# Optimization experiments

Measured on AMD Instinct MI355X. Metric: run time of the kernel, lower is better.

Reference implementation:

```python
import jax, jax.numpy as jnp
import numpy as np
from jax import lax

BETA = 0.95
THRESHOLD = 1.0
B, T, D_IN, D_OUT = 128, 512, 512, 512


def setup_inputs() -> dict:
    key = jax.random.key(0)
    k1, k2, k3 = jax.random.split(key, 3)
    x_seq = jax.random.normal(k1, (B, T, D_IN), dtype=jnp.float32)
    W = jax.random.normal(k2, (D_OUT, D_IN), dtype=jnp.float32) * (1.0 / np.sqrt(D_IN))
    b = jax.random.normal(k3, (D_OUT,), dtype=jnp.float32) * 0.01
    return {"x_seq": x_seq, "W": W, "b": b}


def reference(x_seq, W, b):
    # Batch the linear across all timesteps: [B,T,D_in] @ [D_out,D_in]^T -> [B,T,D_out]
    currents = jnp.einsum('bti,oi->bto', x_seq, W) + b

    def step(mem, cur):  # mem: [B, D_out], cur: [B, D_out]
        mem = BETA * mem + cur
        spk = (mem > THRESHOLD).astype(mem.dtype)
        return mem - spk * THRESHOLD, spk

    mem0 = jnp.zeros((x_seq.shape[0], W.shape[0]), dtype=x_seq.dtype)
    _, spikes_tbd = lax.scan(step, mem0, jnp.swapaxes(currents, 0, 1))  # [T,B,D]
    spikes = jnp.swapaxes(spikes_tbd, 0, 1)  # [B,T,D]
    return spikes, spikes.sum()
```

## Files before the change

### kernel.cpp

```cpp
#include <hip/hip_runtime.h>
#include <hip/hip_bf16.h>

#define M_TOT 65536
#define K_DIM 512
#define N_DIM 512
#define T_STEPS 512
#define BETA 0.95f

#define BM 128
#define BN 128
#define BK 64

typedef __attribute__((ext_vector_type(8))) short bf16x8;
typedef __attribute__((ext_vector_type(4))) float f32x4;

static __device__ __forceinline__ unsigned short f2bf(float f) {
    __hip_bfloat16 h = __float2bfloat16(f);
    return __builtin_bit_cast(unsigned short, h);
}

__global__ __launch_bounds__(256) void gemm_currents(
    const float* __restrict__ X,
    const float* __restrict__ W,
    const float* __restrict__ bias,
    float* __restrict__ C)
{
    __shared__ unsigned short Xs[BM][BK];
    __shared__ unsigned short Ws[BN][BK];

    const int lin  = blockIdx.x;
    const int swz  = (lin & 7) * 256 + (lin >> 3);
    const int mtile = swz >> 2;
    const int ntile = swz & 3;

    const int tid  = threadIdx.x;
    const int lane = tid & 63;
    const int wave = tid >> 6;
    const int wr = wave >> 1;
    const int wc = wave & 1;

    const int row0 = mtile * BM;
    const int col0 = ntile * BN;

    f32x4 acc[4][4] = {};

    const int sr0 = tid >> 4;
    const int skg = (tid & 15) << 2;

    for (int k0 = 0; k0 < K_DIM; k0 += BK) {
        #pragma unroll
        for (int i = 0; i < 8; ++i) {
            int r  = sr0 + i * 16;
            int kgs = skg ^ ((r & 7) << 3);
            float4 xv = *(const float4*)(X + (size_t)(row0 + r) * K_DIM + k0 + skg);
            float4 wv = *(const float4*)(W + (size_t)(col0 + r) * K_DIM + k0 + skg);
            ushort4 xb, wb;
            xb.x = f2bf(xv.x); xb.y = f2bf(xv.y); xb.z = f2bf(xv.z); xb.w = f2bf(xv.w);
            wb.x = f2bf(wv.x); wb.y = f2bf(wv.y); wb.z = f2bf(wv.z); wb.w = f2bf(wv.w);
            *(ushort4*)(&Xs[r][kgs]) = xb;
            *(ushort4*)(&Ws[r][kgs]) = wb;
        }
        __syncthreads();

        const int frow = lane & 15;
        const int cblk = lane >> 4;
        #pragma unroll
        for (int kh = 0; kh < 2; ++kh) {
            bf16x8 afr[4], bfr[4];
            #pragma unroll
            for (int m = 0; m < 4; ++m) {
                int row = wr * 64 + m * 16 + frow;
                int c = (kh * 4 + cblk) ^ (row & 7);
                afr[m] = *(const bf16x8*)(&Xs[row][c * 8]);
            }
            #pragma unroll
            for (int n = 0; n < 4; ++n) {
                int row = wc * 64 + n * 16 + frow;
                int c = (kh * 4 + cblk) ^ (row & 7);
                bfr[n] = *(const bf16x8*)(&Ws[row][c * 8]);
            }
            #pragma unroll
            for (int m = 0; m < 4; ++m)
                #pragma unroll
                for (int n = 0; n < 4; ++n)
                    acc[m][n] = __builtin_amdgcn_mfma_f32_16x16x32_bf16(
                        afr[m], bfr[n], acc[m][n], 0, 0, 0);
        }
        __syncthreads();
    }

    const int crow_base = (lane >> 4) * 4;
    const int ccol = lane & 15;
    #pragma unroll
    for (int n = 0; n < 4; ++n) {
        int col = col0 + wc * 64 + n * 16 + ccol;
        float bv = bias[col];
        #pragma unroll
        for (int m = 0; m < 4; ++m) {
            int rowb = row0 + wr * 64 + m * 16 + crow_base;
            #pragma unroll
            for (int r = 0; r < 4; ++r) {
                C[(size_t)(rowb + r) * N_DIM + col] = acc[m][n][r] + bv;
            }
        }
    }
}

__global__ void zero_sum(float* s) { *s = 0.0f; }

__global__ __launch_bounds__(256) void lif_scan(
    float* __restrict__ C,
    float* __restrict__ sum_out)
{
    const int idx = blockIdx.x * 256 + threadIdx.x;
    float* p = C + (size_t)(idx >> 9) * (T_STEPS * N_DIM) + (idx & 511);

    float mem = 0.0f;
    int count = 0;
    float a[8], b[8];

    #pragma unroll
    for (int j = 0; j < 8; ++j)
        a[j] = __builtin_nontemporal_load(p + (size_t)j * N_DIM);

    for (int t = 0; t < T_STEPS; t += 16) {
        #pragma unroll
        for (int j = 0; j < 8; ++j)
            b[j] = __builtin_nontemporal_load(p + (size_t)(t + 8 + j) * N_DIM);
        #pragma unroll
        for (int j = 0; j < 8; ++j) {
            mem = BETA * mem + a[j];
            float spk = (mem > 1.0f) ? 1.0f : 0.0f;
            mem -= spk;
            __builtin_nontemporal_store(spk, p + (size_t)(t + j) * N_DIM);
            count += (int)spk;
        }
        if (t + 16 < T_STEPS) {
            #pragma unroll
            for (int j = 0; j < 8; ++j)
                a[j] = __builtin_nontemporal_load(p + (size_t)(t + 16 + j) * N_DIM);
        }
        #pragma unroll
        for (int j = 0; j < 8; ++j) {
            mem = BETA * mem + b[j];
            float spk = (mem > 1.0f) ? 1.0f : 0.0f;
            mem -= spk;
            __builtin_nontemporal_store(spk, p + (size_t)(t + 8 + j) * N_DIM);
            count += (int)spk;
        }
    }

    #pragma unroll
    for (int off = 32; off > 0; off >>= 1)
        count += __shfl_down(count, off);
    __shared__ int wsum[4];
    if ((threadIdx.x & 63) == 0) wsum[threadIdx.x >> 6] = count;
    __syncthreads();
    if (threadIdx.x == 0) {
        int tot = wsum[0] + wsum[1] + wsum[2] + wsum[3];
        atomicAdd(sum_out, (float)tot);
    }
}

extern "C" void kernel_launch(void* const* d_in, const int* in_sizes, int n_in,
                              void* d_out, int out_size, void* d_ws, size_t ws_size,
                              hipStream_t stream) {
    const float* X    = (const float*)d_in[0];
    const float* W    = (const float*)d_in[1];
    const float* bias = (const float*)d_in[2];
    float* out = (float*)d_out;

    gemm_currents<<<(M_TOT / BM) * (N_DIM / BN), 256, 0, stream>>>(X, W, bias, out);
    zero_sum<<<1, 1, 0, stream>>>(out + (size_t)M_TOT * N_DIM);
    lif_scan<<<M_TOT / 256, 256, 0, stream>>>(out, out + (size_t)M_TOT * N_DIM);
}
```

Baseline: 333.3 us.

## Double-buffer GEMM LDS tiles with register prefetch, fold sum zeroing, deepen scan prefetch

The GEMM now keeps two LDS buffers. The next K tile is loaded from global into registers while MFMAs run on the current buffer, which removes one barrier per iteration and hides load latency. Zeroing of the sum slot moves into the GEMM kernel, dropping a separate launch. The LIF scan prefetches 16 timesteps per half instead of 8 and uses plain loads instead of nontemporal ones. The cost is higher register and LDS use, and launch_bounds(256,2) may constrain allocation.

```diff
diff --git a/kernel.cpp b/kernel.cpp
--- a/kernel.cpp
+++ b/kernel.cpp
@@ -19,14 +19,31 @@
     return __builtin_bit_cast(unsigned short, h);
 }
 
-__global__ __launch_bounds__(256) void gemm_currents(
+static __device__ __forceinline__ void stage_tiles(
+    unsigned short (*__restrict__ Xs)[BK], unsigned short (*__restrict__ Ws)[BK],
+    const float4* xr, const float4* wv, int sr0, int skg)
+{
+    #pragma unroll
+    for (int i = 0; i < 8; ++i) {
+        int r   = sr0 + i * 16;
+        int kgs = skg ^ ((r & 7) << 3);
+        ushort4 xb, wb;
+        xb.x = f2bf(xr[i].x); xb.y = f2bf(xr[i].y); xb.z = f2bf(xr[i].z); xb.w = f2bf(xr[i].w);
+        wb.x = f2bf(wv[i].x); wb.y = f2bf(wv[i].y); wb.z = f2bf(wv[i].z); wb.w = f2bf(wv[i].w);
+        *(ushort4*)(&Xs[r][kgs]) = xb;
+        *(ushort4*)(&Ws[r][kgs]) = wb;
+    }
+}
+
+__global__ __launch_bounds__(256, 2) void gemm_currents(
     const float* __restrict__ X,
     const float* __restrict__ W,
     const float* __restrict__ bias,
-    float* __restrict__ C)
+    float* __restrict__ C,
+    float* __restrict__ sum_out)
 {
-    __shared__ unsigned short Xs[BM][BK];
-    __shared__ unsigned short Ws[BN][BK];
+    __shared__ unsigned short Xs[2][BM][BK];
+    __shared__ unsigned short Ws[2][BN][BK];
 
     const int lin  = blockIdx.x;
     const int swz  = (lin & 7) * 256 + (lin >> 3);
@@ -39,6 +56,8 @@
     const int wr = wave >> 1;
     const int wc = wave & 1;
 
+    if (lin == 0 && tid == 0) *sum_out = 0.0f;
+
     const int row0 = mtile * BM;
     const int col0 = ntile * BN;
 
@@ -46,24 +65,37 @@
 
     const int sr0 = tid >> 4;
     const int skg = (tid & 15) << 2;
-
-    for (int k0 = 0; k0 < K_DIM; k0 += BK) {
-        #pragma unroll
-        for (int i = 0; i < 8; ++i) {
-            int r  = sr0 + i * 16;
-            int kgs = skg ^ ((r & 7) << 3);
-            float4 xv = *(const float4*)(X + (size_t)(row0 + r) * K_DIM + k0 + skg);
-            float4 wv = *(const float4*)(W + (size_t)(col0 + r) * K_DIM + k0 + skg);
-            ushort4 xb, wb;
-            xb.x = f2bf(xv.x); xb.y = f2bf(xv.y); xb.z = f2bf(xv.z); xb.w = f2bf(xv.w);
-            wb.x = f2bf(wv.x); wb.y = f2bf(wv.y); wb.z = f2bf(wv.z); wb.w = f2bf(wv.w);
-            *(ushort4*)(&Xs[r][kgs]) = xb;
-            *(ushort4*)(&Ws[r][kgs]) = wb;
-        }
+    const float* xbase = X + (size_t)row0 * K_DIM + skg;
+    const float* wbase = W + (size_t)col0 * K_DIM + skg;
+
+    float4 xr[8], wv[8];
+
+    #pragma unroll
+    for (int i = 0; i < 8; ++i) {
+        int r = sr0 + i * 16;
+        xr[i] = *(const float4*)(xbase + (size_t)r * K_DIM);
+        wv[i] = *(const float4*)(wbase + (size_t)r * K_DIM);
+    }
+    stage_tiles(Xs[0], Ws[0], xr, wv, sr0, skg);
+
+    const int frow = lane & 15;
+    const int cblk = lane >> 4;
+
+    for (int t = 0; t < 8; ++t) {
         __syncthreads();
 
-        const int frow = lane & 15;
-        const int cblk = lane >> 4;
+        if (t < 7) {
+            const int k0n = (t + 1) * BK;
+            #pragma unroll
+            for (int i = 0; i < 8; ++i) {
+                int r = sr0 + i * 16;
+                xr[i] = *(const float4*)(xbase + (size_t)r * K_DIM + k0n);
+                wv[i] = *(const float4*)(wbase + (size_t)r * K_DIM + k0n);
+            }
+        }
+
+        unsigned short (*Xb)[BK] = Xs[t & 1];
+        unsigned short (*Wb)[BK] = Ws[t & 1];
         #pragma unroll
         for (int kh = 0; kh < 2; ++kh) {
             bf16x8 afr[4], bfr[4];
@@ -71,13 +103,13 @@
             for (int m = 0; m < 4; ++m) {
                 int row = wr * 64 + m * 16 + frow;
                 int c = (kh * 4 + cblk) ^ (row & 7);
-                afr[m] = *(const bf16x8*)(&Xs[row][c * 8]);
+                afr[m] = *(const bf16x8*)(&Xb[row][c * 8]);
             }
             #pragma unroll
             for (int n = 0; n < 4; ++n) {
                 int row = wc * 64 + n * 16 + frow;
                 int c = (kh * 4 + cblk) ^ (row & 7);
-                bfr[n] = *(const bf16x8*)(&Ws[row][c * 8]);
+                bfr[n] = *(const bf16x8*)(&Wb[row][c * 8]);
             }
             #pragma unroll
             for (int m = 0; m < 4; ++m)
@@ -86,7 +118,9 @@
                     acc[m][n] = __builtin_amdgcn_mfma_f32_16x16x32_bf16(
                         afr[m], bfr[n], acc[m][n], 0, 0, 0);
         }
-        __syncthreads();
+
+        if (t < 7)
+            stage_tiles(Xs[(t + 1) & 1], Ws[(t + 1) & 1], xr, wv, sr0, skg);
     }
 
     const int crow_base = (lane >> 4) * 4;
@@ -105,8 +139,6 @@
         }
     }
 }
-
-__global__ void zero_sum(float* s) { *s = 0.0f; }
 
 __global__ __launch_bounds__(256) void lif_scan(
     float* __restrict__ C,
@@ -117,35 +149,35 @@
 
     float mem = 0.0f;
     int count = 0;
-    float a[8], b[8];
-
-    #pragma unroll
-    for (int j = 0; j < 8; ++j)
-        a[j] = __builtin_nontemporal_load(p + (size_t)j * N_DIM);
-
-    for (int t = 0; t < T_STEPS; t += 16) {
-        #pragma unroll
-        for (int j = 0; j < 8; ++j)
-            b[j] = __builtin_nontemporal_load(p + (size_t)(t + 8 + j) * N_DIM);
-        #pragma unroll
-        for (int j = 0; j < 8; ++j) {
+    float a[16], b[16];
+
+    #pragma unroll
+    for (int j = 0; j < 16; ++j)
+        a[j] = p[(size_t)j * N_DIM];
+
+    for (int t = 0; t < T_STEPS; t += 32) {
+        #pragma unroll
+        for (int j = 0; j < 16; ++j)
+            b[j] = p[(size_t)(t + 16 + j) * N_DIM];
+        #pragma unroll
+        for (int j = 0; j < 16; ++j) {
             mem = BETA * mem + a[j];
             float spk = (mem > 1.0f) ? 1.0f : 0.0f;
             mem -= spk;
             __builtin_nontemporal_store(spk, p + (size_t)(t + j) * N_DIM);
             count += (int)spk;
         }
-        if (t + 16 < T_STEPS) {
-            #pragma unroll
-            for (int j = 0; j < 8; ++j)
-                a[j] = __builtin_nontemporal_load(p + (size_t)(t + 16 + j) * N_DIM);
-        }
-        #pragma unroll
-        for (int j = 0; j < 8; ++j) {
+        if (t + 32 < T_STEPS) {
+            #pragma unroll
+            for (int j = 0; j < 16; ++j)
+                a[j] = p[(size_t)(t + 32 + j) * N_DIM];
+        }
+        #pragma unroll
+        for (int j = 0; j < 16; ++j) {
             mem = BETA * mem + b[j];
             float spk = (mem > 1.0f) ? 1.0f : 0.0f;
             mem -= spk;
-            __builtin_nontemporal_store(spk, p + (size_t)(t + 8 + j) * N_DIM);
+            __builtin_nontemporal_store(spk, p + (size_t)(t + 16 + j) * N_DIM);
             count += (int)spk;
         }
     }
@@ -169,8 +201,8 @@
     const float* W    = (const float*)d_in[1];
     const float* bias = (const float*)d_in[2];
     float* out = (float*)d_out;
-
-    gemm_currents<<<(M_TOT / BM) * (N_DIM / BN), 256, 0, stream>>>(X, W, bias, out);
-    zero_sum<<<1, 1, 0, stream>>>(out + (size_t)M_TOT * N_DIM);
-    lif_scan<<<M_TOT / 256, 256, 0, stream>>>(out, out + (size_t)M_TOT * N_DIM);
-}
+    float* sum_slot = out + (size_t)M_TOT * N_DIM;
+
+    gemm_currents<<<(M_TOT / BM) * (N_DIM / BN), 256, 0, stream>>>(X, W, bias, out, sum_slot);
+    lif_scan<<<M_TOT / 256, 256, 0, stream>>>(out, sum_slot);
+}
```

Result: no change. 333.5 us (+0.1%).
